# Performance work log

Measured on AMD Instinct MI355X. Metric: run time of the kernel, lower is better.

## Reference

```python
import jax, jax.numpy as jnp
import numpy as np

EPS = 1e-08
KERNEL = 3


def setup_inputs() -> dict:
    key = jax.random.key(0)
    k1, k2, k3, k4 = jax.random.split(key, 4)
    N, IN_CH, OUT_CH, H, W, STYLE_DIM = 16, 256, 256, 64, 64, 512
    x = jax.random.normal(k1, (N, IN_CH, H, W), dtype=jnp.float32)
    style = jax.random.normal(k2, (N, STYLE_DIM), dtype=jnp.float32)
    # base weight: [1, out_ch, in_ch, k, k] (torch.randn init)
    weight = jax.random.normal(k3, (1, OUT_CH, IN_CH, KERNEL, KERNEL), dtype=jnp.float32)
    # modulation Linear(style_dim -> in_ch): weight ~ N(0,1), bias = 0
    mod_w = jax.random.normal(k4, (IN_CH, STYLE_DIM), dtype=jnp.float32)
    mod_b = jnp.zeros((IN_CH,), dtype=jnp.float32)
    return {"x": x, "style": style, "weight": weight, "mod_w": mod_w, "mod_b": mod_b}


def _per_sample_conv(xi, wi):
    # xi: [in_ch, H, W], wi: [out_ch, in_ch, k, k]
    pad = KERNEL // 2
    out = jax.lax.conv_general_dilated(
        xi[None], wi,
        window_strides=(1, 1),
        padding=[(pad, pad), (pad, pad)],
        dimension_numbers=("NCHW", "OIHW", "NCHW"),
    )
    return out[0]  # [out_ch, H, W]


def reference(x, style, weight, mod_w, mod_b):
    # modulation: Linear(style) -> [N, in_ch]
    s = style @ mod_w.T + mod_b  # [N, in_ch]
    # modulate base weight: [N, out_ch, in_ch, k, k]
    w = weight * (s[:, None, :, None, None] + 1.0)
    # demodulate
    demod = jax.lax.rsqrt(jnp.sum(w * w, axis=(2, 3, 4)) + EPS)  # [N, out_ch]
    w = w * demod[:, :, None, None, None]
    # grouped conv with groups=N == per-sample conv, vmapped over batch
    out = jax.vmap(_per_sample_conv)(x, w)  # [N, out_ch, H, W]
    return out
```

## Files before the change

kernel.cpp:

```cpp
#include <hip/hip_runtime.h>
#include <hip/hip_bf16.h>
#include <stdint.h>


#define NB  16
#define IC  256
#define OC  256
#define HW  64
#define HWP 66
#define SD  512
#define SPATIAL 4096

typedef __hip_bfloat16 bf16;
typedef __bf16 bf16x8 __attribute__((ext_vector_type(8)));
typedef float  f32x4  __attribute__((ext_vector_type(4)));
typedef uint32_t u32a3 __attribute__((address_space(3)));
typedef const uint32_t u32a1 __attribute__((address_space(1)));

static __device__ __forceinline__ unsigned short f2bu(float f) {
    bf16 h = __float2bfloat16(f);
    union { bf16 b; unsigned short u; } c; c.b = h; return c.u;
}
static __device__ __forceinline__ void gll16(const void* g, void* l) {
    __builtin_amdgcn_global_load_lds((u32a1*)g, (u32a3*)l, 16, 0, 0);
}

__global__ __launch_bounds__(256)
void k_prep1(const float* __restrict__ weight, const float* __restrict__ style,
             const float* __restrict__ mod_w, const float* __restrict__ mod_b,
             float* __restrict__ wsq, bf16* __restrict__ wt2,
             uint4* __restrict__ xs4, float* __restrict__ scale) {
    int b = blockIdx.x, t = threadIdx.x;
    if (b < 256) {
        int tid = b * 256 + t;
        const float* wp = weight + (size_t)tid * 9;
        float v[9], s = 0.f;
        #pragma unroll
        for (int r = 0; r < 9; ++r) { v[r] = wp[r]; s += v[r] * v[r]; }
        wsq[tid] = s;
        #pragma unroll
        for (int r = 0; r < 9; ++r) wt2[(r << 16) + tid] = __float2bfloat16(v[r]);
    } else if (b < 784) {
        int idx = b - 256;
        int n = idx / 33, bx = idx - n * 33;
        int f = bx * 256 + t;
        int u = f >> 5, q = f & 31;
        if (u >= 260) return;
        int rb;
        if      (u <  66) rb = u;
        else if (u < 132) rb = 65 * 66 + (u - 66);
        else if (u < 196) rb = (u - 131) * 66;
        else              rb = (u - 195) * 66 + 65;
        xs4[(size_t)n * 139392 + rb * 32 + q] = make_uint4(0u, 0u, 0u, 0u);
    } else {
        int lane = t & 63;
        int w = (b - 784) * 4 + (t >> 6);
        int n = w >> 8, ic = w & 255;
        const float4* mw4 = (const float4*)mod_w + (size_t)ic * 128 + lane * 2;
        const float4* st4 = (const float4*)style + (size_t)n * 128 + lane * 2;
        float4 a0 = mw4[0], a1 = mw4[1], s0 = st4[0], s1 = st4[1];
        float acc = a0.x*s0.x + a0.y*s0.y + a0.z*s0.z + a0.w*s0.w
                  + a1.x*s1.x + a1.y*s1.y + a1.z*s1.z + a1.w*s1.w;
        #pragma unroll
        for (int off = 32; off > 0; off >>= 1) acc += __shfl_down(acc, off);
        if (lane == 0) scale[w] = acc + mod_b[ic] + 1.0f;
    }
}

__global__ __launch_bounds__(256)
void k_prep2(const float* __restrict__ x, const float* __restrict__ scale,
             const float* __restrict__ wsq, bf16* __restrict__ xs,
             float* __restrict__ demod) {
    __shared__ unsigned short tile[HW * 264];
    int b = blockIdx.x, t = threadIdx.x;
    if (b < 1024) {
        int y = b & 63, n = b >> 6;
        const float* sc = scale + n * IC;
        const float4* xp4 = (const float4*)(x + ((size_t)n * IC) * SPATIAL + (size_t)y * HW);
        #pragma unroll
        for (int i = 0; i < 16; ++i) {
            int fid = i * 256 + t;
            int ic = fid >> 4, f4 = fid & 15;
            float4 v = xp4[(size_t)ic * 1024 + f4];
            float s = sc[ic];
            int sp = f4 * 4;
            tile[(sp + 0) * 264 + ic] = f2bu(v.x * s);
            tile[(sp + 1) * 264 + ic] = f2bu(v.y * s);
            tile[(sp + 2) * 264 + ic] = f2bu(v.z * s);
            tile[(sp + 3) * 264 + ic] = f2bu(v.w * s);
        }
        __syncthreads();
        uint4* dst4 = (uint4*)(xs + (((size_t)n * HWP + (y + 1)) * HWP + 1) * IC);
        #pragma unroll
        for (int j = 0; j < 8; ++j) {
            int uid = j * 256 + t;
            int sp = uid >> 5, g = uid & 31;
            dst4[sp * 32 + g] = *(const uint4*)&tile[sp * 264 + g * 8];
        }
    } else {
        int n = b - 1024, oc = t;
        float* sc = (float*)tile;
        sc[t] = scale[n * IC + t];
        __syncthreads();
        const float4* wp4 = (const float4*)(wsq + (size_t)oc * IC);
        const float4* sc4 = (const float4*)sc;
        float acc = 0.f;
        #pragma unroll 8
        for (int i = 0; i < 64; ++i) {
            float4 q = wp4[i], s = sc4[i];
            acc += q.x*s.x*s.x + q.y*s.y*s.y + q.z*s.z*s.z + q.w*s.w*s.w;
        }
        demod[n * OC + oc] = rsqrtf(acc + 1e-8f);
    }
}

__global__ __launch_bounds__(256, 4)
void k_conv(const bf16* __restrict__ xs, const bf16* __restrict__ wt2,
            const float* __restrict__ demod, float* __restrict__ out) {
    __shared__ unsigned short Al[128 * 64];
    __shared__ unsigned short Bl[128 * 64];
    int t = threadIdx.x, l = t & 63, w = t >> 6;
    int wm = w & 1, wn = w >> 1;
    int bid = blockIdx.x;
    int work = ((bid & 7) << 7) | (bid >> 3);
    int bn = work & 1, st = work >> 1;
    int n = st >> 5;
    int sp_base = (st & 31) << 7;
    int oc_base = bn << 7;

    int lrow = l >> 3;
    int lseg = (l & 7) ^ lrow;
    int sp0 = sp_base + w * 32 + lrow;
    const bf16* gA0 = xs + (((size_t)n * HWP + (sp0 >> 6)) * HWP + (sp0 & 63)) * IC + lseg * 8;
    const bf16* gB0 = wt2 + (size_t)(oc_base + w * 32 + lrow) * IC + lseg * 8;
    char* Ab = (char*)Al + w * 4096;
    char* Bb = (char*)Bl + w * 4096;

    f32x4 acc[4][4];
    #pragma unroll
    for (int i = 0; i < 4; ++i)
        #pragma unroll
        for (int j = 0; j < 4; ++j) acc[i][j] = (f32x4){0.f, 0.f, 0.f, 0.f};

    int rAbase = (wm * 64 + (l & 15)) * 64;
    int rBbase = (wn * 64 + (l & 15)) * 64;
    int q0 = l >> 4, xk = l & 7;

    for (int ch = 0; ch < 36; ++ch) {
        int r = ch >> 2;
        int ic0 = (ch & 3) << 6;
        int ky = r / 3, kx = r - ky * 3;
        int aoff = (ky * HWP + kx) * IC + ic0;
        int boff = (r << 16) + ic0;
        __syncthreads();
        #pragma unroll
        for (int i = 0; i < 4; ++i)
            gll16(gA0 + aoff + i * 2048, Ab + i * 1024);
        #pragma unroll
        for (int i = 0; i < 4; ++i)
            gll16(gB0 + boff + i * 2048, Bb + i * 1024);
        __syncthreads();
        #pragma unroll
        for (int kk = 0; kk < 2; ++kk) {
            int ks = (((kk << 2) + q0) ^ xk) << 3;
            bf16x8 af[4], bfr[4];
            #pragma unroll
            for (int mi = 0; mi < 4; ++mi)
                af[mi] = *reinterpret_cast<const bf16x8*>(&Al[rAbase + mi * 1024 + ks]);
            #pragma unroll
            for (int ni = 0; ni < 4; ++ni)
                bfr[ni] = *reinterpret_cast<const bf16x8*>(&Bl[rBbase + ni * 1024 + ks]);
            #pragma unroll
            for (int mi = 0; mi < 4; ++mi)
                #pragma unroll
                for (int ni = 0; ni < 4; ++ni)
                    acc[mi][ni] = __builtin_amdgcn_mfma_f32_16x16x32_bf16(
                        af[mi], bfr[ni], acc[mi][ni], 0, 0, 0);
        }
    }

    const float* dm = demod + n * OC;
    int ocol = l & 15, orow = (l >> 4) << 2;
    #pragma unroll
    for (int ni = 0; ni < 4; ++ni) {
        int oc = oc_base + wn * 64 + ni * 16 + ocol;
        float d = dm[oc];
        size_t ob = ((size_t)(n * OC + oc)) * SPATIAL + sp_base + wm * 64 + orow;
        #pragma unroll
        for (int mi = 0; mi < 4; ++mi) {
            f32x4 a = acc[mi][ni];
            f32x4 o = { a[0] * d, a[1] * d, a[2] * d, a[3] * d };
            *reinterpret_cast<f32x4*>(out + ob + mi * 16) = o;
        }
    }
}

extern "C" void kernel_launch(void* const* d_in, const int* in_sizes, int n_in,
                              void* d_out, int out_size, void* d_ws, size_t ws_size,
                              hipStream_t stream) {
    const float* x      = (const float*)d_in[0];
    const float* style  = (const float*)d_in[1];
    const float* weight = (const float*)d_in[2];
    const float* mod_w  = (const float*)d_in[3];
    const float* mod_b  = (const float*)d_in[4];
    float* out = (float*)d_out;

    char* ws = (char*)d_ws;
    float* scale = (float*)(ws + 0);
    float* demod = (float*)(ws + 16384);
    float* wsq   = (float*)(ws + 32768);
    bf16*  wt2   = (bf16*)(ws + 294912);
    bf16*  xs    = (bf16*)(ws + 1474560);

    k_prep1<<<1808, 256, 0, stream>>>(weight, style, mod_w, mod_b,
                                      wsq, wt2, (uint4*)xs, scale);
    k_prep2<<<1040, 256, 0, stream>>>(x, scale, wsq, xs, demod);
    k_conv<<<1024, 256, 0, stream>>>(xs, wt2, demod, out);
}
```

Before: 202.7 us.

## Rewrite conv GEMM as 256x256 tile with double-buffered LDS pipeline

```diff
diff --git a/kernel.cpp b/kernel.cpp
--- a/kernel.cpp
+++ b/kernel.cpp
@@ -10,6 +10,7 @@
 #define HWP 66
 #define SD  512
 #define SPATIAL 4096
+#define HWPIC 16896
 
 typedef __hip_bfloat16 bf16;
 typedef __bf16 bf16x8 __attribute__((ext_vector_type(8)));
@@ -71,7 +72,7 @@
 void k_prep2(const float* __restrict__ x, const float* __restrict__ scale,
              const float* __restrict__ wsq, bf16* __restrict__ xs,
              float* __restrict__ demod) {
-    __shared__ unsigned short tile[HW * 264];
+    __shared__ unsigned short tile[HW * 256];
     int b = blockIdx.x, t = threadIdx.x;
     if (b < 1024) {
         int y = b & 63, n = b >> 6;
@@ -83,11 +84,12 @@
             int ic = fid >> 4, f4 = fid & 15;
             float4 v = xp4[(size_t)ic * 1024 + f4];
             float s = sc[ic];
-            int sp = f4 * 4;
-            tile[(sp + 0) * 264 + ic] = f2bu(v.x * s);
-            tile[(sp + 1) * 264 + ic] = f2bu(v.y * s);
-            tile[(sp + 2) * 264 + ic] = f2bu(v.z * s);
-            tile[(sp + 3) * 264 + ic] = f2bu(v.w * s);
+            int sp = f4 << 2;
+            int sw = ic ^ ((f4 & 7) << 3);
+            tile[(sp + 0) * 256 + sw] = f2bu(v.x * s);
+            tile[(sp + 1) * 256 + sw] = f2bu(v.y * s);
+            tile[(sp + 2) * 256 + sw] = f2bu(v.z * s);
+            tile[(sp + 3) * 256 + sw] = f2bu(v.w * s);
         }
         __syncthreads();
         uint4* dst4 = (uint4*)(xs + (((size_t)n * HWP + (y + 1)) * HWP + 1) * IC);
@@ -95,7 +97,8 @@
         for (int j = 0; j < 8; ++j) {
             int uid = j * 256 + t;
             int sp = uid >> 5, g = uid & 31;
-            dst4[sp * 32 + g] = *(const uint4*)&tile[sp * 264 + g * 8];
+            dst4[sp * 32 + g] =
+                *(const uint4*)&tile[sp * 256 + ((g ^ ((sp >> 2) & 7)) << 3)];
         }
     } else {
         int n = b - 1024, oc = t;
@@ -114,83 +117,128 @@
     }
 }
 
-__global__ __launch_bounds__(256, 4)
+#define VM4 asm volatile("s_waitcnt vmcnt(4)" ::: "memory")
+#define VM2 asm volatile("s_waitcnt vmcnt(2)" ::: "memory")
+#define VM0 asm volatile("s_waitcnt vmcnt(0)" ::: "memory")
+#define BAR __builtin_amdgcn_s_barrier()
+
+__global__ __launch_bounds__(512, 2)
 void k_conv(const bf16* __restrict__ xs, const bf16* __restrict__ wt2,
             const float* __restrict__ demod, float* __restrict__ out) {
-    __shared__ unsigned short Al[128 * 64];
-    __shared__ unsigned short Bl[128 * 64];
+    extern __shared__ char smem[];
     int t = threadIdx.x, l = t & 63, w = t >> 6;
     int wm = w & 1, wn = w >> 1;
     int bid = blockIdx.x;
-    int work = ((bid & 7) << 7) | (bid >> 3);
-    int bn = work & 1, st = work >> 1;
-    int n = st >> 5;
-    int sp_base = (st & 31) << 7;
-    int oc_base = bn << 7;
-
-    int lrow = l >> 3;
-    int lseg = (l & 7) ^ lrow;
-    int sp0 = sp_base + w * 32 + lrow;
-    const bf16* gA0 = xs + (((size_t)n * HWP + (sp0 >> 6)) * HWP + (sp0 & 63)) * IC + lseg * 8;
-    const bf16* gB0 = wt2 + (size_t)(oc_base + w * 32 + lrow) * IC + lseg * 8;
-    char* Ab = (char*)Al + w * 4096;
-    char* Bb = (char*)Bl + w * 4096;
-
-    f32x4 acc[4][4];
+    int work = ((bid & 7) << 5) | (bid >> 3);
+    int nimg = work >> 4;
+    int ybase = (work & 15) << 2;
+    int spb = (work & 15) << 8;
+
+    int srow = (w << 3) + (l >> 3);
+    int gseg = (l & 7) ^ (l >> 3);
+    const bf16* gA = xs + (((size_t)nimg * HWP + ybase) * HWP + srow) * IC + (gseg << 3);
+    const bf16* gB = wt2 + ((size_t)srow << 8) + (gseg << 3);
+    int stW = w << 10;
+
+    int aRow = ((wm << 6) + (l & 15)) << 7;
+    int bRow = ((wn << 5) + (l & 15)) << 7;
+    int sg0 = ((l >> 4) ^ (l & 7)) << 4;
+    int sg1 = sg0 ^ 64;
+
+    f32x4 acc[4][4][2];
     #pragma unroll
-    for (int i = 0; i < 4; ++i)
-        #pragma unroll
-        for (int j = 0; j < 4; ++j) acc[i][j] = (f32x4){0.f, 0.f, 0.f, 0.f};
-
-    int rAbase = (wm * 64 + (l & 15)) * 64;
-    int rBbase = (wn * 64 + (l & 15)) * 64;
-    int q0 = l >> 4, xk = l & 7;
-
-    for (int ch = 0; ch < 36; ++ch) {
-        int r = ch >> 2;
-        int ic0 = (ch & 3) << 6;
-        int ky = r / 3, kx = r - ky * 3;
-        int aoff = (ky * HWP + kx) * IC + ic0;
-        int boff = (r << 16) + ic0;
-        __syncthreads();
-        #pragma unroll
-        for (int i = 0; i < 4; ++i)
-            gll16(gA0 + aoff + i * 2048, Ab + i * 1024);
-        #pragma unroll
-        for (int i = 0; i < 4; ++i)
-            gll16(gB0 + boff + i * 2048, Bb + i * 1024);
-        __syncthreads();
-        #pragma unroll
-        for (int kk = 0; kk < 2; ++kk) {
-            int ks = (((kk << 2) + q0) ^ xk) << 3;
-            bf16x8 af[4], bfr[4];
+    for (int p = 0; p < 4; ++p)
+        #pragma unroll
+        for (int m = 0; m < 4; ++m)
             #pragma unroll
-            for (int mi = 0; mi < 4; ++mi)
-                af[mi] = *reinterpret_cast<const bf16x8*>(&Al[rAbase + mi * 1024 + ks]);
-            #pragma unroll
-            for (int ni = 0; ni < 4; ++ni)
-                bfr[ni] = *reinterpret_cast<const bf16x8*>(&Bl[rBbase + ni * 1024 + ks]);
-            #pragma unroll
-            for (int mi = 0; mi < 4; ++mi)
-                #pragma unroll
-                for (int ni = 0; ni < 4; ++ni)
-                    acc[mi][ni] = __builtin_amdgcn_mfma_f32_16x16x32_bf16(
-                        af[mi], bfr[ni], acc[mi][ni], 0, 0, 0);
-        }
-    }
-
-    const float* dm = demod + n * OC;
+            for (int n = 0; n < 2; ++n) acc[p][m][n] = (f32x4){0.f, 0.f, 0.f, 0.f};
+
+    bf16x8 af[4][2], bf0[2][2], bf1[2][2];
+
+#define STG_A(ha, PARN, AOFF) do {                                          \
+    const bf16* s_ = gA + (AOFF) + (ha) * 2 * HWPIC;                        \
+    char* d_ = smem + (PARN) * 32768 + (ha) * 16384 + stW;                  \
+    gll16(s_, d_); gll16(s_ + HWPIC, d_ + 8192); } while (0)
+#define STG_B(hb, PARN, BOFF) do {                                          \
+    const bf16* s_ = gB + (BOFF) + (hb) * (128 * IC);                       \
+    char* d_ = smem + 65536 + (PARN) * 32768 + (hb) * 16384 + stW;          \
+    gll16(s_, d_); gll16(s_ + 64 * IC, d_ + 8192); } while (0)
+#define LD_A(QA) do { const char* Ab_ = Ap + (QA) * 16384 + aRow;           \
+    _Pragma("unroll") for (int m_ = 0; m_ < 4; ++m_) {                      \
+        af[m_][0] = *(const bf16x8*)(Ab_ + m_ * 2048 + sg0);                \
+        af[m_][1] = *(const bf16x8*)(Ab_ + m_ * 2048 + sg1); } } while (0)
+#define LD_B(DST, QB) do { const char* Bb_ = Bp + (QB) * 16384 + bRow;      \
+    _Pragma("unroll") for (int n_ = 0; n_ < 2; ++n_) {                      \
+        DST[n_][0] = *(const bf16x8*)(Bb_ + n_ * 2048 + sg0);               \
+        DST[n_][1] = *(const bf16x8*)(Bb_ + n_ * 2048 + sg1); } } while (0)
+#define MM(P, BF) do {                                                      \
+    __builtin_amdgcn_s_setprio(1);                                          \
+    _Pragma("unroll") for (int kk_ = 0; kk_ < 2; ++kk_)                     \
+    _Pragma("unroll") for (int m_ = 0; m_ < 4; ++m_)                        \
+    _Pragma("unroll") for (int n_ = 0; n_ < 2; ++n_)                        \
+        acc[P][m_][n_] = __builtin_amdgcn_mfma_f32_16x16x32_bf16(           \
+            af[m_][kk_], BF[n_][kk_], acc[P][m_][n_], 0, 0, 0);             \
+    __builtin_amdgcn_s_setprio(0); } while (0)
+
+    STG_A(0, 0, 0);
+    STG_B(0, 0, 0);
+    STG_B(1, 0, 0);
+    STG_A(1, 0, 0);
+    VM4;
+    BAR;
+
+    #pragma clang loop unroll(disable)
+    for (int T = 0; T < 35; ++T) {
+        int par = T & 1, parn = par ^ 1;
+        const char* Ap = smem + par * 32768;
+        const char* Bp = smem + 65536 + par * 32768;
+        int Tn = T + 1;
+        int rn = Tn >> 2, icn = (Tn & 3) << 6;
+        int kyn = rn / 3, kxn = rn - kyn * 3;
+        int aoffN = (kyn * HWP + kxn) * IC + icn;
+        int boffN = (rn << 16) + icn;
+
+        LD_A(0); LD_B(bf0, 0);
+        STG_A(0, parn, aoffN);
+        BAR; MM(0, bf0); VM4; BAR;
+        LD_B(bf1, 1);
+        STG_B(0, parn, boffN);
+        BAR; MM(1, bf1); VM4; BAR;
+        LD_A(1);
+        STG_B(1, parn, boffN);
+        BAR; MM(2, bf1); BAR;
+        STG_A(1, parn, aoffN);
+        BAR; MM(3, bf0); VM4; BAR;
+    }
+    {
+        const char* Ap = smem + 32768;
+        const char* Bp = smem + 65536 + 32768;
+        LD_A(0); LD_B(bf0, 0);
+        MM(0, bf0); VM2; BAR;
+        LD_B(bf1, 1);
+        MM(1, bf1); VM0; BAR;
+        LD_A(1);
+        MM(2, bf1);
+        MM(3, bf0);
+    }
+
+    const float* dm = demod + nimg * OC;
     int ocol = l & 15, orow = (l >> 4) << 2;
     #pragma unroll
-    for (int ni = 0; ni < 4; ++ni) {
-        int oc = oc_base + wn * 64 + ni * 16 + ocol;
-        float d = dm[oc];
-        size_t ob = ((size_t)(n * OC + oc)) * SPATIAL + sp_base + wm * 64 + orow;
-        #pragma unroll
-        for (int mi = 0; mi < 4; ++mi) {
-            f32x4 a = acc[mi][ni];
-            f32x4 o = { a[0] * d, a[1] * d, a[2] * d, a[3] * d };
-            *reinterpret_cast<f32x4*>(out + ob + mi * 16) = o;
+    for (int p = 0; p < 4; ++p) {
+        int qa = p >> 1, qb = qa ^ (p & 1);
+        #pragma unroll
+        for (int n = 0; n < 2; ++n) {
+            int oc = (qb << 7) + (wn << 5) + (n << 4) + ocol;
+            float d = dm[oc];
+            size_t ob = ((size_t)(nimg * OC + oc)) * SPATIAL
+                      + spb + (qa << 7) + (wm << 6) + orow;
+            #pragma unroll
+            for (int m = 0; m < 4; ++m) {
+                f32x4 a = acc[p][m][n];
+                f32x4 o = { a[0] * d, a[1] * d, a[2] * d, a[3] * d };
+                *reinterpret_cast<f32x4*>(out + ob + m * 16) = o;
+            }
         }
     }
 }
@@ -212,8 +260,15 @@
     bf16*  wt2   = (bf16*)(ws + 294912);
     bf16*  xs    = (bf16*)(ws + 1474560);
 
+    static int s_attr = 0;
+    if (!s_attr) {
+        hipFuncSetAttribute(reinterpret_cast<const void*>(k_conv),
+                            hipFuncAttributeMaxDynamicSharedMemorySize, 131072);
+        s_attr = 1;
+    }
+
     k_prep1<<<1808, 256, 0, stream>>>(weight, style, mod_w, mod_b,
                                       wsq, wt2, (uint4*)xs, scale);
     k_prep2<<<1040, 256, 0, stream>>>(x, scale, wsq, xs, demod);
-    k_conv<<<1024, 256, 0, stream>>>(xs, wt2, demod, out);
-}
+    k_conv<<<256, 512, 131072, stream>>>(xs, wt2, demod, out);
+}
```

New measurement: 190.2 us. 6.2% less time.
